# Kernel optimization log

Measured on AMD Instinct MI355X. Metric: run time of the kernel, lower is better.

## Reference

```python
import jax, jax.numpy as jnp
import numpy as np

B, N, D, R, STEPS = 16, 512, 512, 8, 2


def setup_inputs() -> dict:
    key = jax.random.key(0)
    ks = jax.random.split(key, 8)
    nodes = jax.random.normal(ks[0], (B, N, D), dtype=jnp.float32)
    edges = jax.random.uniform(ks[1], (B, R, N, N), dtype=jnp.float32)
    scale = 1.0 / np.sqrt(D)
    # per-relation Linear layers: weight [out,in] torch-style, bias [out]
    msg_W = jax.random.uniform(ks[2], (R, D, D), minval=-scale, maxval=scale, dtype=jnp.float32)
    msg_b = jax.random.uniform(ks[3], (R, D), minval=-scale, maxval=scale, dtype=jnp.float32)
    # GRUCell params, gate order (r, z, n) like torch
    w_ih = jax.random.uniform(ks[4], (3 * D, D), minval=-scale, maxval=scale, dtype=jnp.float32)
    w_hh = jax.random.uniform(ks[5], (3 * D, D), minval=-scale, maxval=scale, dtype=jnp.float32)
    b_ih = jax.random.uniform(ks[6], (3 * D,), minval=-scale, maxval=scale, dtype=jnp.float32)
    b_hh = jax.random.uniform(ks[7], (3 * D,), minval=-scale, maxval=scale, dtype=jnp.float32)
    return {"nodes": nodes, "edges": edges, "msg_W": msg_W, "msg_b": msg_b,
            "w_ih": w_ih, "w_hh": w_hh, "b_ih": b_ih, "b_hh": b_hh}


def reference(nodes, edges, msg_W, msg_b, w_ih, w_hh, b_ih, b_hh):
    # nodes: [b,n,d], edges: [b,R,n,n]
    h = nodes  # keep [b,n,d]; torch flattens to [b*n,d] but math is identical
    bias_sum = msg_b.sum(axis=0)  # sum of per-relation biases, [d]
    for _ in range(STEPS):
        # per-relation message passing: m[b,r,i,d] = edges[b,r] @ h[b]
        m = jnp.einsum('brij,bjd->brid', edges, h)
        # per-relation Linear (y = x @ W_r^T + b_r), summed over relations
        agg = jnp.einsum('brid,red->bie', m, msg_W) + bias_sum  # [b,n,d]
        # GRUCell update (gate order r, z, n)
        gi = agg @ w_ih.T + b_ih  # [b,n,3d]
        gh = h @ w_hh.T + b_hh    # [b,n,3d]
        ir, iz, i_n = jnp.split(gi, 3, axis=-1)
        hr, hz, h_n = jnp.split(gh, 3, axis=-1)
        r = jax.nn.sigmoid(ir + hr)
        z = jax.nn.sigmoid(iz + hz)
        n_t = jnp.tanh(i_n + r * h_n)
        h = (1.0 - z) * n_t + z * h
    return h.mean(axis=1)  # [b,d]
```

## Files before the change

### kernel.cpp

```cpp
#include <hip/hip_runtime.h>

typedef _Float16 f16;
typedef __attribute__((ext_vector_type(8))) _Float16 half8;
typedef __attribute__((ext_vector_type(4))) float f32x4;

struct f16x4 { f16 a, b, c, d; };


__device__ __forceinline__ void stage16(const f16* g, f16* l) {
  __builtin_amdgcn_global_load_lds(
      (const __attribute__((address_space(1))) void*)g,
      (__attribute__((address_space(3))) void*)l, 16, 0, 0);
}

__global__ void cvt_fr(const float* __restrict__ in, f16* __restrict__ hi,
                       f16* __restrict__ lo, int n_units) {
  const int u = blockIdx.x * blockDim.x + threadIdx.x;
  if (u >= n_units) return;
  const int l = u & 63, kc = (u >> 6) & 15, rt = u >> 10;
  const long ibase = (long)(rt * 16 + (l & 15)) * 512 + kc * 32 + ((l >> 4) << 3);
  const float4 v0 = *(const float4*)(in + ibase);
  const float4 v1 = *(const float4*)(in + ibase + 4);
  const float v[8] = {v0.x, v0.y, v0.z, v0.w, v1.x, v1.y, v1.z, v1.w};
  half8 h, lw;
#pragma unroll
  for (int e = 0; e < 8; ++e) {
    h[e] = (f16)v[e];
    lw[e] = (f16)(v[e] - (float)h[e]);
  }
  *(half8*)(hi + (long)u * 8) = h;
  *(half8*)(lo + (long)u * 8) = lw;
}

__global__ void cvt_fr1(const float* __restrict__ in, f16* __restrict__ hi,
                        int n_units) {
  const int u = blockIdx.x * blockDim.x + threadIdx.x;
  if (u >= n_units) return;
  const int l = u & 63, kc = (u >> 6) & 15, rt = u >> 10;
  const long ibase = (long)(rt * 16 + (l & 15)) * 512 + kc * 32 + ((l >> 4) << 3);
  const float4 v0 = *(const float4*)(in + ibase);
  const float4 v1 = *(const float4*)(in + ibase + 4);
  const float v[8] = {v0.x, v0.y, v0.z, v0.w, v1.x, v1.y, v1.z, v1.w};
  half8 h;
#pragma unroll
  for (int e = 0; e < 8; ++e) h[e] = (f16)v[e];
  *(half8*)(hi + (long)u * 8) = h;
}

__global__ void bias_sum_k(const float* __restrict__ msg_b, float* __restrict__ bs) {
  int e = threadIdx.x;
  float s = 0.f;
  for (int r = 0; r < 8; ++r) s += msg_b[r * 512 + e];
  bs[e] = s;
}

template <int SA, int SB, int OUT, int SWZ>
__global__ __launch_bounds__(256, 3) void gemm_dr(
    const f16* __restrict__ Ah, const f16* __restrict__ Al,
    const f16* __restrict__ Bh, const f16* __restrict__ Bl,
    f16* __restrict__ Chi, f16* __restrict__ Clo, float* __restrict__ Cf,
    const float* __restrict__ bias, int N, int R, long sAr, long sBr,
    int zdiv, long sAzr, long sAzb, long sBzr, long sBzb,
    long sCzr, long sCzb) {
  constexpr int NU = 8 * ((1 + SA) + (1 + SB));
  constexpr int NW = NU / 4;
  constexpr int BUF = NU * 512;
  constexpr int SMEMN = (2 * BUF > 16384) ? 2 * BUF : 16384;
  __shared__ __align__(16) f16 smem[SMEMN];

  const int tid = threadIdx.x;
  int bx, by, z;
  if constexpr (SWZ) {
    const int l = blockIdx.x;
    const int xcd = l & 7, m2 = l >> 3, zq = m2 >> 4, t = m2 & 15;
    z = (zq << 3) | xcd; bx = t & 3; by = t >> 2;
  } else {
    bx = blockIdx.x; by = blockIdx.y; z = blockIdx.z;
  }
  const int zr = z % zdiv, zb = z / zdiv;
  const int lane = tid & 63;
  const int w = tid >> 6;
  const int wm = (w & 1) << 6;
  const int wn = (w >> 1) << 6;

  const f16* gA = Ah + (long)zr * sAzr + (long)zb * sAzb + (long)by * 65536 + lane * 8;
  const f16* gB = Bh + (long)zr * sBzr + (long)zb * sBzb + (long)bx * 65536 + lane * 8;
  const f16* gAl = SA ? (Al + (gA - Ah)) : nullptr;
  const f16* gBl = SB ? (Bl + (gB - Bh)) : nullptr;
  const long cbase = (long)zr * sCzr + (long)zb * sCzb;

  f32x4 acc[4][4];
#pragma unroll
  for (int i = 0; i < 4; ++i)
#pragma unroll
    for (int j = 0; j < 4; ++j) acc[i][j] = (f32x4){0.f, 0.f, 0.f, 0.f};

  const int NIT = R * 16;

  auto ST = [&](int bf, int ii) {
    const long oa = (long)(ii >> 4) * sAr + (ii & 15) * 512;
    const long ob = (long)(ii >> 4) * sBr + (ii & 15) * 512;
    f16* lb = &smem[bf * BUF];
#pragma unroll
    for (int q = 0; q < NW; ++q) {
      const int s = w * NW + q;
      const f16* src;
      if (s < 8) {
        src = gA + (long)s * 8192 + oa;
      } else if (SA && s < 16) {
        src = gAl + (long)(s - 8) * 8192 + oa;
      } else {
        const int sb = s - 8 * (1 + SA);
        src = (SB && sb >= 8) ? (gBl + (long)(sb - 8) * 8192 + ob)
                              : (gB + (long)sb * 8192 + ob);
      }
      stage16(src, lb + s * 512);
    }
  };

  auto CP = [&](int bf) {
    const f16* lb = &smem[bf * BUF];
    const int lo8 = lane * 8;
    half8 bh[4], bl[4];
#pragma unroll
    for (int nt = 0; nt < 4; ++nt) {
      const int ub = 8 * (1 + SA) + (w >> 1) * 4 + nt;
      bh[nt] = *(const half8*)(lb + ub * 512 + lo8);
      if constexpr (SB) bl[nt] = *(const half8*)(lb + (ub + 8) * 512 + lo8);
    }
#pragma unroll
    for (int mt = 0; mt < 4; ++mt) {
      const int ua = (w & 1) * 4 + mt;
      const half8 ah = *(const half8*)(lb + ua * 512 + lo8);
      half8 al;
      if constexpr (SA) al = *(const half8*)(lb + (ua + 8) * 512 + lo8);
#pragma unroll
      for (int nt = 0; nt < 4; ++nt) {
        acc[mt][nt] = __builtin_amdgcn_mfma_f32_16x16x32_f16(
            ah, bh[nt], acc[mt][nt], 0, 0, 0);
        if constexpr (SB)
          acc[mt][nt] = __builtin_amdgcn_mfma_f32_16x16x32_f16(
              ah, bl[nt], acc[mt][nt], 0, 0, 0);
        if constexpr (SA)
          acc[mt][nt] = __builtin_amdgcn_mfma_f32_16x16x32_f16(
              al, bh[nt], acc[mt][nt], 0, 0, 0);
      }
    }
  };

  auto WAITN = [&]() {
    if constexpr (NW == 4)      asm volatile("s_waitcnt vmcnt(4)" ::: "memory");
    else if constexpr (NW == 6) asm volatile("s_waitcnt vmcnt(6)" ::: "memory");
    else if constexpr (NW == 8) asm volatile("s_waitcnt vmcnt(8)" ::: "memory");
    else                        asm volatile("s_waitcnt vmcnt(0)" ::: "memory");
  };

  ST(0, 0);
  ST(1, 1);
  int cur = 0;
  for (int t = 0; t < NIT; ++t) {
    if (t < NIT - 1) WAITN();
    else asm volatile("s_waitcnt vmcnt(0)" ::: "memory");
    __builtin_amdgcn_s_barrier();
    __builtin_amdgcn_sched_barrier(0);
    CP(cur);
    asm volatile("s_waitcnt lgkmcnt(0)" ::: "memory");
    __builtin_amdgcn_s_barrier();
    if (t + 2 < NIT) ST(cur, t + 2);
    cur ^= 1;
  }
  __syncthreads();

  const int l15 = lane & 15;
  const int rb = (lane >> 4) << 2;
  if constexpr (OUT) {
#pragma unroll
    for (int nt = 0; nt < 4; ++nt) {
      const int col = wn + nt * 16 + l15;
#pragma unroll
      for (int mt = 0; mt < 4; ++mt)
#pragma unroll
        for (int v = 0; v < 4; ++v) {
          const int row = wm + mt * 16 + rb + v;
          const float cval = acc[mt][nt][v];
          const f16 h = (f16)cval;
          smem[row * 128 + ((col >> 3) ^ (row & 15)) * 8 + (col & 7)] = h;
          acc[mt][nt][v] = cval - (float)h;
        }
    }
    __syncthreads();
#pragma unroll
    for (int i2 = 0; i2 < 8; ++i2) {
      const int u = i2 * 256 + tid;
      const int ul = u & 63, kc_loc = (u >> 6) & 3, rt_loc = u >> 8;
      const int row = rt_loc * 16 + (ul & 15);
      const int gcol = kc_loc * 4 + (ul >> 4);
      const int4 vv = *(const int4*)&smem[row * 128 + ((gcol ^ (row & 15)) << 3)];
      *(int4*)&Chi[cbase + ((long)(by * 8 + rt_loc) * 16 + bx * 4 + kc_loc) * 512 + ul * 8] = vv;
    }
    __syncthreads();
#pragma unroll
    for (int nt = 0; nt < 4; ++nt) {
      const int col = wn + nt * 16 + l15;
#pragma unroll
      for (int mt = 0; mt < 4; ++mt)
#pragma unroll
        for (int v = 0; v < 4; ++v) {
          const int row = wm + mt * 16 + rb + v;
          smem[row * 128 + ((col >> 3) ^ (row & 15)) * 8 + (col & 7)] = (f16)acc[mt][nt][v];
        }
    }
    __syncthreads();
#pragma unroll
    for (int i2 = 0; i2 < 8; ++i2) {
      const int u = i2 * 256 + tid;
      const int ul = u & 63, kc_loc = (u >> 6) & 3, rt_loc = u >> 8;
      const int row = rt_loc * 16 + (ul & 15);
      const int gcol = kc_loc * 4 + (ul >> 4);
      const int4 vv = *(const int4*)&smem[row * 128 + ((gcol ^ (row & 15)) << 3)];
      *(int4*)&Clo[cbase + ((long)(by * 8 + rt_loc) * 16 + bx * 4 + kc_loc) * 512 + ul * 8] = vv;
    }
  } else {
#pragma unroll
    for (int nt = 0; nt < 4; ++nt) {
      const int col = bx * 128 + wn + nt * 16 + l15;
      const float bv = bias ? bias[col] : 0.f;
#pragma unroll
      for (int mt = 0; mt < 4; ++mt) {
        const long rowbase = (long)(by * 128 + wm + mt * 16 + rb) * N + col;
#pragma unroll
        for (int v = 0; v < 4; ++v)
          Cf[cbase + rowbase + (long)v * N] = acc[mt][nt][v] + bv;
      }
    }
  }
}

__global__ void reduce_agg4(const f16* __restrict__ Phi, const f16* __restrict__ Plo,
                            const float* __restrict__ bsum,
                            f16* __restrict__ hi, f16* __restrict__ lo) {
  const long i = ((long)blockIdx.x * blockDim.x + threadIdx.x) * 4;
  const int li = (int)i;
  const int l = (li >> 3) & 63, kc = (li >> 9) & 15;
  const int e0 = kc * 32 + ((l >> 4) << 3) + (li & 4);
  const float4 b = *(const float4*)(bsum + e0);
  float v0 = b.x, v1 = b.y, v2 = b.z, v3 = b.w;
#pragma unroll
  for (int q = 0; q < 4; ++q) {
    const long o = (long)q * 4194304 + i;
    const f16x4 ph = *(const f16x4*)(Phi + o);
    const f16x4 pl = *(const f16x4*)(Plo + o);
    v0 += (float)ph.a + (float)pl.a;
    v1 += (float)ph.b + (float)pl.b;
    v2 += (float)ph.c + (float)pl.c;
    v3 += (float)ph.d + (float)pl.d;
  }
  f16x4 h, lw;
  h.a = (f16)v0; lw.a = (f16)(v0 - (float)h.a);
  h.b = (f16)v1; lw.b = (f16)(v1 - (float)h.b);
  h.c = (f16)v2; lw.c = (f16)(v2 - (float)h.c);
  h.d = (f16)v3; lw.d = (f16)(v3 - (float)h.d);
  *(f16x4*)(hi + i) = h;
  *(f16x4*)(lo + i) = lw;
}

__global__ void gru_k(const float* __restrict__ gi, const float* __restrict__ gh,
                      const float* __restrict__ holdf, f16* __restrict__ hhi) {
  const int u = blockIdx.x * blockDim.x + threadIdx.x;
  const int row = u >> 6, d0 = (u & 63) << 3;
  const long gbase = (long)row * 1536 + d0;
  const float4 giR0 = *(const float4*)(gi + gbase),      giR1 = *(const float4*)(gi + gbase + 4);
  const float4 giZ0 = *(const float4*)(gi + gbase + 512), giZ1 = *(const float4*)(gi + gbase + 516);
  const float4 giN0 = *(const float4*)(gi + gbase + 1024), giN1 = *(const float4*)(gi + gbase + 1028);
  const float4 ghR0 = *(const float4*)(gh + gbase),      ghR1 = *(const float4*)(gh + gbase + 4);
  const float4 ghZ0 = *(const float4*)(gh + gbase + 512), ghZ1 = *(const float4*)(gh + gbase + 516);
  const float4 ghN0 = *(const float4*)(gh + gbase + 1024), ghN1 = *(const float4*)(gh + gbase + 1028);
  const float irv[8] = {giR0.x, giR0.y, giR0.z, giR0.w, giR1.x, giR1.y, giR1.z, giR1.w};
  const float izv[8] = {giZ0.x, giZ0.y, giZ0.z, giZ0.w, giZ1.x, giZ1.y, giZ1.z, giZ1.w};
  const float inv[8] = {giN0.x, giN0.y, giN0.z, giN0.w, giN1.x, giN1.y, giN1.z, giN1.w};
  const float hrv[8] = {ghR0.x, ghR0.y, ghR0.z, ghR0.w, ghR1.x, ghR1.y, ghR1.z, ghR1.w};
  const float hzv[8] = {ghZ0.x, ghZ0.y, ghZ0.z, ghZ0.w, ghZ1.x, ghZ1.y, ghZ1.z, ghZ1.w};
  const float hnv[8] = {ghN0.x, ghN0.y, ghN0.z, ghN0.w, ghN1.x, ghN1.y, ghN1.z, ghN1.w};
  const long hflat = (long)(row >> 4) * 8192 + (d0 >> 5) * 512 +
                     ((row & 15) + (((d0 >> 3) & 3) << 4)) * 8;
  half8 hh8;
  if (!holdf) hh8 = *(const half8*)(hhi + hflat);
  half8 oh;
#pragma unroll
  for (int e = 0; e < 8; ++e) {
    const float h = holdf ? holdf[(long)row * 512 + d0 + e] : (float)hh8[e];
    const float r = 1.f / (1.f + __expf(-(irv[e] + hrv[e])));
    const float zg = 1.f / (1.f + __expf(-(izv[e] + hzv[e])));
    const float nt = tanhf(inv[e] + r * hnv[e]);
    const float o = (1.f - zg) * nt + zg * h;
    oh[e] = (f16)o;
  }
  *(half8*)(hhi + hflat) = oh;
}

__global__ void mean_k(const f16* __restrict__ hhi, float* __restrict__ out) {
  const int b = blockIdx.x;
  const int d = threadIdx.x;
  const long base = (long)b * 262144 + (d >> 5) * 512 + (((d >> 3) & 3) << 4) * 8 + (d & 7);
  float s = 0.f;
  for (int n = 0; n < 512; ++n) {
    const long j = base + (long)(n >> 4) * 8192 + (n & 15) * 8;
    s += (float)hhi[j];
  }
  out[b * 512 + d] = s * (1.f / 512.f);
}

extern "C" void kernel_launch(void* const* d_in, const int* in_sizes, int n_in,
                              void* d_out, int out_size, void* d_ws, size_t ws_size,
                              hipStream_t stream) {
  const float* nodes = (const float*)d_in[0];
  const float* edges = (const float*)d_in[1];
  const float* msg_W = (const float*)d_in[2];
  const float* msg_b = (const float*)d_in[3];
  const float* w_ih  = (const float*)d_in[4];
  const float* w_hh  = (const float*)d_in[5];
  const float* b_ih  = (const float*)d_in[6];
  const float* b_hh  = (const float*)d_in[7];
  float* out = (float*)d_out;

  char* ws = (char*)d_ws;
  size_t off = 0;
  auto alloc = [&](size_t bytes) -> char* {
    char* p = ws + off;
    off += (bytes + 1023) & ~(size_t)1023;
    return p;
  };
  f16* edges_hi = (f16*)alloc(33554432ull * 2);
  f16* W_hi     = (f16*)alloc(2097152ull * 2);
  f16* W_lo     = (f16*)alloc(2097152ull * 2);
  f16* wih_hi   = (f16*)alloc(786432ull * 2);
  f16* whh_hi   = (f16*)alloc(786432ull * 2);
  f16* h_hi     = (f16*)alloc(4194304ull * 2);
  f16* hWT_hi   = (f16*)alloc(33554432ull * 2);
  f16* hWT_lo   = (f16*)alloc(33554432ull * 2);
  f16* Phi      = (f16*)alloc(16777216ull * 2);
  f16* Plo      = (f16*)alloc(16777216ull * 2);
  float* bsum   = (float*)alloc(512 * 4);
  float* gi = (float*)hWT_hi;
  float* gh = (float*)hWT_lo;
  f16* agg_hi = hWT_hi + 25165824;
  f16* agg_lo = agg_hi + 4194304;

  cvt_fr1<<<16384, 256, 0, stream>>>(edges, edges_hi, 4194304);
  cvt_fr<<<1024,  256, 0, stream>>>(msg_W, W_hi, W_lo, 262144);
  cvt_fr1<<<384,  256, 0, stream>>>(w_ih, wih_hi, 98304);
  cvt_fr1<<<384,  256, 0, stream>>>(w_hh, whh_hi, 98304);
  cvt_fr1<<<2048, 256, 0, stream>>>(nodes, h_hi, 524288);
  bias_sum_k<<<1, 512, 0, stream>>>(msg_b, bsum);

  for (int step = 0; step < 2; ++step) {
    gemm_dr<1, 0, 1, 0><<<dim3(4, 4, 128), 256, 0, stream>>>(
        W_hi, W_lo, h_hi, nullptr, hWT_hi, hWT_lo, nullptr, nullptr,
        512, 1, 0L, 0L, 8, 262144L, 0L, 0L, 262144L, 262144L, 2097152L);
    gemm_dr<0, 1, 1, 1><<<dim3(1024, 1, 1), 256, 0, stream>>>(
        edges_hi, nullptr, hWT_hi, hWT_lo, Phi, Plo, nullptr, nullptr,
        512, 2, 262144L, 262144L, 4, 524288L, 2097152L, 524288L, 2097152L,
        4194304L, 262144L);
    reduce_agg4<<<4096, 256, 0, stream>>>(Phi, Plo, bsum, agg_hi, agg_lo);
    gemm_dr<1, 0, 0, 0><<<dim3(12, 64, 1), 256, 0, stream>>>(
        agg_hi, agg_lo, wih_hi, nullptr, nullptr, nullptr, gi, b_ih,
        1536, 1, 0L, 0L, 1, 0L, 0L, 0L, 0L, 0L, 0L);
    gemm_dr<0, 0, 0, 0><<<dim3(12, 64, 1), 256, 0, stream>>>(
        h_hi, nullptr, whh_hi, nullptr, nullptr, nullptr, gh, b_hh,
        1536, 1, 0L, 0L, 1, 0L, 0L, 0L, 0L, 0L, 0L);
    gru_k<<<2048, 256, 0, stream>>>(gi, gh, step ? nullptr : nodes, h_hi);
  }
  mean_k<<<16, 512, 0, stream>>>(h_hi, out);
}
```

Before: 746.2 us.

## Add 8-wave triple-buffered 256x256 GEMM kernel for message-passing products

Introduces gemm_8ph, a 512-thread kernel with 256x256 output tiles, a three-stage LDS ring fed by global_load_lds, and MFMA work split into four phases that interleave the next stage's loads with setprio and barriers. It also maps blocks to XCDs by hand and writes hi/lo split fp16 outputs through a swizzled LDS staging area. It replaces the two gemm_dr launches for W·h and edges·hWT, aiming to raise MFMA utilization and overlap memory with compute. The cost is heavy register and LDS use, which limits occupancy, plus complex hand-written wait counts that could be fragile.

```diff
diff --git a/kernel.cpp b/kernel.cpp
--- a/kernel.cpp
+++ b/kernel.cpp
@@ -52,6 +52,183 @@
   float s = 0.f;
   for (int r = 0; r < 8; ++r) s += msg_b[r * 512 + e];
   bs[e] = s;
+}
+
+template <int SPL>
+__global__ __launch_bounds__(512, 2) void gemm_8ph(
+    const f16* __restrict__ Ah, const f16* __restrict__ Lo,
+    const f16* __restrict__ Bh, f16* __restrict__ Chi, f16* __restrict__ Clo,
+    int NIT, long sAr, int zdiv, int zpx,
+    long sAzr, long sAzb, long sBzr, long sBzb, long sCzr, long sCzb) {
+  __shared__ __align__(16) f16 smem[73728];
+  const int tid = threadIdx.x;
+  const int lane = tid & 63;
+  const int w = tid >> 6;
+  const int wr = w & 1;
+  const int wc = w >> 1;
+  const int l = blockIdx.x;
+  const int xcd = l & 7, g = l >> 3;
+  const int z = xcd * zpx + (g >> 2), t4 = g & 3;
+  const int bx = t4 & 1, by = t4 >> 1;
+  const int zr = z % zdiv, zb = z / zdiv;
+
+  const f16* Ab = Ah + (long)zr * sAzr + (long)zb * sAzb + (long)by * 131072 + lane * 8;
+  const f16* Bb = Bh + (long)zr * sBzr + (long)zb * sBzb + (long)bx * 131072 + lane * 8;
+  const f16* Lb = SPL ? (Lo + (Ab - Ah)) : (Lo + (Bb - Bh));
+  const long cbase = (long)zr * sCzr + (long)zb * sCzb;
+
+  const f16* sp[6];
+  int so[6];
+#pragma unroll
+  for (int q = 0; q < 6; ++q) {
+    const int s = w * 6 + q;
+    so[q] = s * 512;
+    sp[q] = (s < 16) ? (Ab + (long)s * 8192)
+          : (s < 32) ? (Bb + (long)(s - 16) * 8192)
+                     : (Lb + (long)(s - 32) * 8192);
+  }
+
+  f32x4 acc[8][4];
+#pragma unroll
+  for (int i = 0; i < 8; ++i)
+#pragma unroll
+    for (int j = 0; j < 4; ++j) acc[i][j] = (f32x4){0.f, 0.f, 0.f, 0.f};
+
+  auto KOFF = [&](int ii) { return (long)(ii >> 4) * sAr + (long)(ii & 15) * 512; };
+
+#pragma unroll
+  for (int q = 0; q < 6; ++q) stage16(sp[q] + KOFF(0), &smem[so[q]]);
+  {
+    const long k1 = KOFF(1);
+#pragma unroll
+    for (int q = 0; q < 6; ++q) stage16(sp[q] + k1, &smem[24576 + so[q]]);
+  }
+
+  int cur = 0;
+  const int lo8 = lane * 8;
+  for (int t = 0; t < NIT; ++t) {
+    if (t < NIT - 1) asm volatile("s_waitcnt vmcnt(6)" ::: "memory");
+    else             asm volatile("s_waitcnt vmcnt(0)" ::: "memory");
+    __builtin_amdgcn_s_barrier();
+    __builtin_amdgcn_sched_barrier(0);
+    const f16* lb = &smem[cur * 24576];
+    const bool st = (t + 2 < NIT);
+    int nb = cur + 2; if (nb >= 3) nb -= 3;
+    f16* nd = &smem[nb * 24576];
+    const long nkk = KOFF(st ? t + 2 : 0);
+    half8 bh[4], bl[4];
+#pragma unroll
+    for (int nt = 0; nt < 4; ++nt) {
+      bh[nt] = *(const half8*)(lb + (16 + wc * 4 + nt) * 512 + lo8);
+      if constexpr (!SPL)
+        bl[nt] = *(const half8*)(lb + (32 + wc * 4 + nt) * 512 + lo8);
+    }
+#pragma unroll
+    for (int p = 0; p < 4; ++p) {
+      const int m0 = p * 2;
+      if (st) {
+        if (p == 0)      { stage16(sp[0] + nkk, nd + so[0]); stage16(sp[1] + nkk, nd + so[1]); }
+        else if (p == 1) { stage16(sp[2] + nkk, nd + so[2]); stage16(sp[3] + nkk, nd + so[3]); }
+        else if (p == 2) { stage16(sp[4] + nkk, nd + so[4]); }
+        else             { stage16(sp[5] + nkk, nd + so[5]); }
+      }
+      half8 a0 = *(const half8*)(lb + (wr * 8 + m0) * 512 + lo8);
+      half8 a1 = *(const half8*)(lb + (wr * 8 + m0 + 1) * 512 + lo8);
+      half8 l0, l1;
+      if constexpr (SPL) {
+        l0 = *(const half8*)(lb + (32 + wr * 8 + m0) * 512 + lo8);
+        l1 = *(const half8*)(lb + (32 + wr * 8 + m0 + 1) * 512 + lo8);
+      }
+      __builtin_amdgcn_s_barrier();
+      asm volatile("s_waitcnt lgkmcnt(0)" ::: "memory");
+      __builtin_amdgcn_sched_barrier(0);
+      __builtin_amdgcn_s_setprio(1);
+#pragma unroll
+      for (int nt = 0; nt < 4; ++nt) {
+        acc[m0][nt] = __builtin_amdgcn_mfma_f32_16x16x32_f16(a0, bh[nt], acc[m0][nt], 0, 0, 0);
+        if constexpr (!SPL)
+          acc[m0][nt] = __builtin_amdgcn_mfma_f32_16x16x32_f16(a0, bl[nt], acc[m0][nt], 0, 0, 0);
+        else
+          acc[m0][nt] = __builtin_amdgcn_mfma_f32_16x16x32_f16(l0, bh[nt], acc[m0][nt], 0, 0, 0);
+      }
+#pragma unroll
+      for (int nt = 0; nt < 4; ++nt) {
+        acc[m0 + 1][nt] = __builtin_amdgcn_mfma_f32_16x16x32_f16(a1, bh[nt], acc[m0 + 1][nt], 0, 0, 0);
+        if constexpr (!SPL)
+          acc[m0 + 1][nt] = __builtin_amdgcn_mfma_f32_16x16x32_f16(a1, bl[nt], acc[m0 + 1][nt], 0, 0, 0);
+        else
+          acc[m0 + 1][nt] = __builtin_amdgcn_mfma_f32_16x16x32_f16(l1, bh[nt], acc[m0 + 1][nt], 0, 0, 0);
+      }
+      __builtin_amdgcn_s_setprio(0);
+      __builtin_amdgcn_s_barrier();
+    }
+    cur = cur + 1; if (cur >= 3) cur -= 3;
+  }
+  __syncthreads();
+
+  const int l15 = lane & 15;
+  const int rb = (lane >> 4) << 2;
+#pragma unroll
+  for (int h = 0; h < 2; ++h) {
+    if (wr == h) {
+#pragma unroll
+      for (int nt = 0; nt < 4; ++nt) {
+        const int col = wc * 64 + nt * 16 + l15;
+        const int ch = col >> 7, cl = col & 127;
+#pragma unroll
+        for (int mt = 0; mt < 8; ++mt)
+#pragma unroll
+          for (int v = 0; v < 4; ++v) {
+            const int row = mt * 16 + rb + v;
+            const float cval = acc[mt][nt][v];
+            const f16 hh = (f16)cval;
+            smem[row * 256 + ch * 128 + (((cl >> 3) ^ (row & 15)) << 3) + (cl & 7)] = hh;
+            acc[mt][nt][v] = cval - (float)hh;
+          }
+      }
+    }
+    __syncthreads();
+#pragma unroll
+    for (int i2 = 0; i2 < 8; ++i2) {
+      const int u = i2 * 512 + tid;
+      const int ul = u & 63, kc_loc = (u >> 6) & 7, rt8 = u >> 9;
+      const int row = rt8 * 16 + (ul & 15);
+      const int gc = kc_loc * 4 + (ul >> 4);
+      const int ch = gc >> 4, cl8 = gc & 15;
+      const int4 vv = *(const int4*)&smem[row * 256 + ch * 128 + ((cl8 ^ (row & 15)) << 3)];
+      const long unit = (long)((by * 16 + h * 8 + rt8) * 16 + bx * 8 + kc_loc);
+      *(int4*)&Chi[cbase + unit * 512 + ul * 8] = vv;
+    }
+    __syncthreads();
+    if (wr == h) {
+#pragma unroll
+      for (int nt = 0; nt < 4; ++nt) {
+        const int col = wc * 64 + nt * 16 + l15;
+        const int ch = col >> 7, cl = col & 127;
+#pragma unroll
+        for (int mt = 0; mt < 8; ++mt)
+#pragma unroll
+          for (int v = 0; v < 4; ++v) {
+            const int row = mt * 16 + rb + v;
+            smem[row * 256 + ch * 128 + (((cl >> 3) ^ (row & 15)) << 3) + (cl & 7)] =
+                (f16)acc[mt][nt][v];
+          }
+      }
+    }
+    __syncthreads();
+#pragma unroll
+    for (int i2 = 0; i2 < 8; ++i2) {
+      const int u = i2 * 512 + tid;
+      const int ul = u & 63, kc_loc = (u >> 6) & 7, rt8 = u >> 9;
+      const int row = rt8 * 16 + (ul & 15);
+      const int gc = kc_loc * 4 + (ul >> 4);
+      const int ch = gc >> 4, cl8 = gc & 15;
+      const int4 vv = *(const int4*)&smem[row * 256 + ch * 128 + ((cl8 ^ (row & 15)) << 3)];
+      const long unit = (long)((by * 16 + h * 8 + rt8) * 16 + bx * 8 + kc_loc);
+      *(int4*)&Clo[cbase + unit * 512 + ul * 8] = vv;
+    }
+    __syncthreads();
+  }
 }
 
 template <int SA, int SB, int OUT, int SWZ>
@@ -354,13 +531,12 @@
   bias_sum_k<<<1, 512, 0, stream>>>(msg_b, bsum);
 
   for (int step = 0; step < 2; ++step) {
-    gemm_dr<1, 0, 1, 0><<<dim3(4, 4, 128), 256, 0, stream>>>(
-        W_hi, W_lo, h_hi, nullptr, hWT_hi, hWT_lo, nullptr, nullptr,
-        512, 1, 0L, 0L, 8, 262144L, 0L, 0L, 262144L, 262144L, 2097152L);
-    gemm_dr<0, 1, 1, 1><<<dim3(1024, 1, 1), 256, 0, stream>>>(
-        edges_hi, nullptr, hWT_hi, hWT_lo, Phi, Plo, nullptr, nullptr,
-        512, 2, 262144L, 262144L, 4, 524288L, 2097152L, 524288L, 2097152L,
-        4194304L, 262144L);
+    gemm_8ph<1><<<512, 512, 0, stream>>>(
+        W_hi, W_lo, h_hi, hWT_hi, hWT_lo,
+        16, 0L, 8, 16, 262144L, 0L, 0L, 262144L, 262144L, 2097152L);
+    gemm_8ph<0><<<256, 512, 0, stream>>>(
+        edges_hi, hWT_lo, hWT_hi, Phi, Plo,
+        32, 262144L, 4, 8, 524288L, 2097152L, 524288L, 2097152L, 4194304L, 262144L);
     reduce_agg4<<<4096, 256, 0, stream>>>(Phi, Plo, bsum, agg_hi, agg_lo);
     gemm_dr<1, 0, 0, 0><<<dim3(12, 64, 1), 256, 0, stream>>>(
         agg_hi, agg_lo, wih_hi, nullptr, nullptr, nullptr, gi, b_ih,
```

Measured after the change: 830.1 us. 1.11x slower.
